# Kernel optimization log

Measured on AMD Instinct MI355X. Metric: run time of the kernel, lower is better.

The kernel has to match this reference:

```python
import jax, jax.numpy as jnp
import numpy as np
import math

N = 50000
E = 500000
IN_C = 128
T_FEAT = 16
OUT_C = 128
EPS = 1e-5
NEG_SLOPE = 0.01


def setup_inputs() -> dict:
    key = jax.random.key(0)
    ks = jax.random.split(key, 10)
    x = jax.random.normal(ks[0], (N, IN_C), dtype=jnp.float32)
    edge_index = jax.random.randint(ks[1], (2, E), 0, N, dtype=jnp.int64)
    edge_weight = jax.random.uniform(ks[2], (E,), dtype=jnp.float32)
    time_diff = jax.random.uniform(ks[3], (1,), dtype=jnp.float32)
    d_in = IN_C + T_FEAT
    morning_freq = jax.random.normal(ks[4], (T_FEAT,), dtype=jnp.float32)
    W_gcn = jax.random.normal(ks[5], (d_in, OUT_C), dtype=jnp.float32) / np.sqrt(d_in)
    b_gcn = jnp.zeros((OUT_C,), dtype=jnp.float32)
    gamma = jnp.ones((OUT_C,), dtype=jnp.float32)
    beta = jnp.zeros((OUT_C,), dtype=jnp.float32)
    W_lin = jax.random.normal(ks[6], (OUT_C, OUT_C), dtype=jnp.float32) / np.sqrt(OUT_C)
    b_lin = jax.random.normal(ks[7], (OUT_C,), dtype=jnp.float32) * 0.01
    return {"x": x, "edge_index": edge_index, "edge_weight": edge_weight,
            "time_diff": time_diff, "morning_freq": morning_freq,
            "W_gcn": W_gcn, "b_gcn": b_gcn, "gamma": gamma, "beta": beta,
            "W_lin": W_lin, "b_lin": b_lin}


def _gcn_conv(h, edge_index, edge_weight):
    # PyG GCNConv aggregation: add self-loops (weight 1), symmetric normalization.
    row, col = edge_index[0], edge_index[1]
    loop = jnp.arange(N, dtype=edge_index.dtype)
    row_f = jnp.concatenate([row, loop])
    col_f = jnp.concatenate([col, loop])
    ew_f = jnp.concatenate([edge_weight, jnp.ones((N,), dtype=h.dtype)])
    deg = jax.ops.segment_sum(ew_f, col_f, num_segments=N)
    dinv = jnp.where(deg > 0, jax.lax.rsqrt(jnp.maximum(deg, 1e-12)), 0.0)
    norm = dinv[row_f] * ew_f * dinv[col_f]                 # [E+N]
    msg = h[row_f] * norm[:, None]                          # gather + scale
    return jax.ops.segment_sum(msg, col_f, num_segments=N)  # scatter-add


def reference(x, edge_index, edge_weight, time_diff, morning_freq,
              W_gcn, b_gcn, gamma, beta, W_lin, b_lin):
    td = time_diff[0]
    # time_segment == 'morning_peak': sin encoding, tiled over all nodes
    enc = jnp.sin(td * morning_freq * math.pi)              # [T]
    enc = jnp.broadcast_to(enc[None, :], (x.shape[0], T_FEAT))
    h = jnp.concatenate([x, enc], axis=1)                   # [N, in+T]
    h = h @ W_gcn                                           # GCN linear transform
    h = _gcn_conv(h, edge_index, edge_weight) + b_gcn       # [N, out]
    # BatchNorm1d (training-mode batch statistics, biased variance)
    mean = jnp.mean(h, axis=0)
    var = jnp.mean(jnp.square(h - mean), axis=0)
    h = gamma * (h - mean) * jax.lax.rsqrt(var + EPS) + beta
    h = jnp.where(h >= 0, h, NEG_SLOPE * h)                 # LeakyReLU
    h = h @ W_lin + b_lin                                   # Linear (dropout=eval identity)
    return h
```

## Files before the change

### kernel.cpp

```cpp
#include <hip/hip_runtime.h>
#include <hip/hip_bf16.h>

#define NN 50000
#define NE 500000
#define C 128
#define NBLK ((NN + 255) / 256)
#define SPB (NN / 8)
#define RB 128
#define RROWS ((SPB + RB - 1) / RB)
#define BN_EPS 1e-5f
#define NEG 0.01f
#define WSCALE 16777216.0f
#define WMASK  0xFFFFFFFFFFFULL

__device__ inline unsigned short f2bf(float f) {
    unsigned int u = __float_as_uint(f);
    unsigned int r = (u + 0x7fffu + ((u >> 16) & 1u)) >> 16;
    return (unsigned short)r;
}
__device__ inline float4 bf4_to_f4(uint2 u) {
    float4 r;
    r.x = __uint_as_float(u.x << 16);
    r.y = __uint_as_float(u.x & 0xffff0000u);
    r.z = __uint_as_float(u.y << 16);
    r.w = __uint_as_float(u.y & 0xffff0000u);
    return r;
}

__global__ void zero_kernel(float* __restrict__ p, long n) {
    long i = (long)blockIdx.x * blockDim.x + threadIdx.x;
    long s = (long)gridDim.x * blockDim.x;
    for (; i < n; i += s) p[i] = 0.f;
}

__global__ void cvec_kernel(const float* __restrict__ td, const float* __restrict__ mf,
                            const float* __restrict__ Wg, float* __restrict__ cvec) {
    int o = threadIdx.x;
    float t = td[0];
    float acc = 0.f;
#pragma unroll
    for (int j = 0; j < 16; j++) {
        float s = sinf(t * mf[j] * 3.14159265358979323846f);
        acc = fmaf(s, Wg[(128 + j) * C + o], acc);
    }
    cvec[o] = acc;
}

__global__ __launch_bounds__(256) void gemm1_kernel(const float* __restrict__ X,
                                                    const float* __restrict__ W,
                                                    const float* __restrict__ cvec,
                                                    unsigned short* __restrict__ Hb) {
    __shared__ __align__(16) float At[32][68];
    __shared__ __align__(16) float Bt[32][68];
    const int t = threadIdx.x;
    const int r0 = blockIdx.x * 64;
    const int c0 = blockIdx.y * 64;
    const int tr = t >> 4, tc = t & 15;
    float acc[4][4] = {};
    for (int k0 = 0; k0 < 128; k0 += 32) {
#pragma unroll
        for (int rr = 0; rr < 64; rr += 32) {
            int lr = rr + (t >> 3);
            int r = r0 + lr;
            int kk = (t & 7) * 4;
            float4 v = make_float4(0.f, 0.f, 0.f, 0.f);
            if (r < NN) v = *(const float4*)(X + (size_t)r * C + k0 + kk);
            At[kk + 0][lr] = v.x; At[kk + 1][lr] = v.y;
            At[kk + 2][lr] = v.z; At[kk + 3][lr] = v.w;
        }
#pragma unroll
        for (int kk2 = 0; kk2 < 32; kk2 += 16) {
            int k = kk2 + (t >> 4);
            int c = (t & 15) * 4;
            *(float4*)&Bt[k][c] = *(const float4*)(W + (size_t)(k0 + k) * C + c0 + c);
        }
        __syncthreads();
#pragma unroll
        for (int k = 0; k < 32; k++) {
            float4 a = *(const float4*)&At[k][tr * 4];
            float4 b = *(const float4*)&Bt[k][tc * 4];
            float av[4] = {a.x, a.y, a.z, a.w};
            float bv[4] = {b.x, b.y, b.z, b.w};
#pragma unroll
            for (int i = 0; i < 4; i++)
#pragma unroll
                for (int j = 0; j < 4; j++)
                    acc[i][j] = fmaf(av[i], bv[j], acc[i][j]);
        }
        __syncthreads();
    }
    float4 cv = *(const float4*)(cvec + c0 + tc * 4);
#pragma unroll
    for (int i = 0; i < 4; i++) {
        int r = r0 + tr * 4 + i;
        if (r < NN) {
            uint2 o;
            o.x = (unsigned int)f2bf(acc[i][0] + cv.x) | ((unsigned int)f2bf(acc[i][1] + cv.y) << 16);
            o.y = (unsigned int)f2bf(acc[i][2] + cv.z) | ((unsigned int)f2bf(acc[i][3] + cv.w) << 16);
            *(uint2*)(Hb + (size_t)r * C + c0 + tc * 4) = o;
        }
    }
}

__global__ void hist_kernel(const int* __restrict__ ei, const float* __restrict__ ew,
                            unsigned long long* __restrict__ hist) {
    int e = blockIdx.x * blockDim.x + threadIdx.x;
    if (e < NE) {
        int c = ei[NE + e];
        unsigned long long pack = (1ULL << 44) | (unsigned long long)(ew[e] * WSCALE);
        atomicAdd(&hist[c], pack);
    }
}

__global__ __launch_bounds__(256) void scanp1_kernel(const unsigned long long* __restrict__ hist,
                                                     int* __restrict__ rptr,
                                                     int* __restrict__ bsum) {
    __shared__ int s[256];
    const int t = threadIdx.x;
    const int i = blockIdx.x * 256 + t;
    int v = (i < NN) ? (int)(hist[i] >> 44) : 0;
    s[t] = v;
    __syncthreads();
    for (int off = 1; off < 256; off <<= 1) {
        int add = (t >= off) ? s[t - off] : 0;
        __syncthreads();
        s[t] += add;
        __syncthreads();
    }
    if (i < NN) rptr[i] = s[t] - v;
    if (t == 255) bsum[blockIdx.x] = s[255];
}

__global__ __launch_bounds__(256) void scanp2_kernel(const int* __restrict__ bsum,
                                                     int* __restrict__ boff) {
    __shared__ int s[256];
    const int t = threadIdx.x;
    int v = (t < NBLK) ? bsum[t] : 0;
    s[t] = v;
    __syncthreads();
    for (int off = 1; off < 256; off <<= 1) {
        int add = (t >= off) ? s[t - off] : 0;
        __syncthreads();
        s[t] += add;
        __syncthreads();
    }
    if (t < NBLK) boff[t] = s[t] - v;
}

__global__ void scanp3_kernel(int* __restrict__ rptr, const int* __restrict__ boff,
                              const unsigned long long* __restrict__ hist,
                              int* __restrict__ cursor, float* __restrict__ dinv) {
    int i = blockIdx.x * blockDim.x + threadIdx.x;
    if (i < NN) {
        int rp = rptr[i] + boff[i >> 8];
        rptr[i] = rp;
        cursor[i] = rp;
        float degw = (float)(hist[i] & WMASK) * (1.0f / WSCALE);
        dinv[i] = rsqrtf(degw + 1.0f);
    }
    if (i == 0) rptr[NN] = NE;
}

__global__ void fill_kernel(const int* __restrict__ ei, const float* __restrict__ ew,
                            const float* __restrict__ dinv,
                            int* __restrict__ cursor, int2* __restrict__ csr) {
    int e = blockIdx.x * blockDim.x + threadIdx.x;
    if (e >= NE) return;
    int r = ei[e], c = ei[NE + e];
    int slot = atomicAdd(&cursor[c], 1);
    float w = dinv[r] * ew[e] * dinv[c];
    csr[slot] = make_int2(r, __float_as_int(w));
}

__global__ __launch_bounds__(256) void spmm_kernel(const int* __restrict__ rptr,
                                                   const int2* __restrict__ csr,
                                                   const unsigned short* __restrict__ Hb,
                                                   const float* __restrict__ dinv,
                                                   const float* __restrict__ bg,
                                                   float* __restrict__ OUT,
                                                   float* __restrict__ P) {
    const int nl = threadIdx.x >> 5;
    const int lane = threadIdx.x & 31;
    const int node = blockIdx.x * 8 + nl;
    const int ch = lane * 4;
    int s = rptr[node], e = rptr[node + 1];
    float d = dinv[node];
    float dd = d * d;
    float4 h = bf4_to_f4(*(const uint2*)(Hb + (size_t)node * C + ch));
    float4 acc = make_float4(dd * h.x, dd * h.y, dd * h.z, dd * h.w);
    int j = s;
    for (; j + 2 <= e; j += 2) {
        int2 e0 = csr[j], e1 = csr[j + 1];
        float w0 = __int_as_float(e0.y), w1 = __int_as_float(e1.y);
        float4 v0 = bf4_to_f4(*(const uint2*)(Hb + (size_t)e0.x * C + ch));
        float4 v1 = bf4_to_f4(*(const uint2*)(Hb + (size_t)e1.x * C + ch));
        acc.x = fmaf(v0.x, w0, acc.x); acc.y = fmaf(v0.y, w0, acc.y);
        acc.z = fmaf(v0.z, w0, acc.z); acc.w = fmaf(v0.w, w0, acc.w);
        acc.x = fmaf(v1.x, w1, acc.x); acc.y = fmaf(v1.y, w1, acc.y);
        acc.z = fmaf(v1.z, w1, acc.z); acc.w = fmaf(v1.w, w1, acc.w);
    }
    if (j < e) {
        int2 e0 = csr[j];
        float w0 = __int_as_float(e0.y);
        float4 v0 = bf4_to_f4(*(const uint2*)(Hb + (size_t)e0.x * C + ch));
        acc.x = fmaf(v0.x, w0, acc.x); acc.y = fmaf(v0.y, w0, acc.y);
        acc.z = fmaf(v0.z, w0, acc.z); acc.w = fmaf(v0.w, w0, acc.w);
    }
    float4 b = *(const float4*)(bg + ch);
    acc.x += b.x; acc.y += b.y; acc.z += b.z; acc.w += b.w;
    *(float4*)(OUT + (size_t)node * C + ch) = acc;

    __shared__ __align__(16) float4 sred[2][8][32];
    float4 sq = make_float4(acc.x * acc.x, acc.y * acc.y, acc.z * acc.z, acc.w * acc.w);
    sred[0][nl][lane] = acc;
    sred[1][nl][lane] = sq;
    __syncthreads();
    if (nl == 0) {
        float4 s0 = sred[0][0][lane], q0 = sred[1][0][lane];
#pragma unroll
        for (int k = 1; k < 8; k++) {
            float4 a = sred[0][k][lane];
            float4 q = sred[1][k][lane];
            s0.x += a.x; s0.y += a.y; s0.z += a.z; s0.w += a.w;
            q0.x += q.x; q0.y += q.y; q0.z += q.z; q0.w += q.w;
        }
        float* row = P + (size_t)blockIdx.x * 256;
        *(float4*)(row + ch) = s0;
        *(float4*)(row + 128 + ch) = q0;
    }
}

__global__ __launch_bounds__(256) void reduce1_kernel(const float* __restrict__ P,
                                                      float* __restrict__ P2) {
    const int c = threadIdx.x;
    const int r0 = blockIdx.x * RROWS;
    const int r1 = min(r0 + RROWS, SPB);
    float a0 = 0.f, a1 = 0.f, a2 = 0.f, a3 = 0.f;
    int r = r0;
    for (; r + 4 <= r1; r += 4) {
        a0 += P[(size_t)(r + 0) * 256 + c];
        a1 += P[(size_t)(r + 1) * 256 + c];
        a2 += P[(size_t)(r + 2) * 256 + c];
        a3 += P[(size_t)(r + 3) * 256 + c];
    }
    for (; r < r1; r++) a0 += P[(size_t)r * 256 + c];
    P2[(size_t)blockIdx.x * 256 + c] = (a0 + a1) + (a2 + a3);
}

__global__ void bnparam_kernel(const float* __restrict__ P2,
                               const float* __restrict__ gm, const float* __restrict__ bt,
                               float* __restrict__ sc, float* __restrict__ sh) {
    int c = threadIdx.x;
    float s0 = 0.f, s1 = 0.f, q0 = 0.f, q1 = 0.f;
    for (int k = 0; k < RB; k += 2) {
        s0 += P2[(size_t)k * 256 + c];
        q0 += P2[(size_t)k * 256 + 128 + c];
        s1 += P2[(size_t)(k + 1) * 256 + c];
        q1 += P2[(size_t)(k + 1) * 256 + 128 + c];
    }
    float ssum = s0 + s1, ssq = q0 + q1;
    float mean = ssum / (float)NN;
    float var = ssq / (float)NN - mean * mean;
    var = fmaxf(var, 0.f);
    float r = rsqrtf(var + BN_EPS);
    float s = gm[c] * r;
    sc[c] = s;
    sh[c] = bt[c] - mean * s;
}

__global__ __launch_bounds__(256) void final_kernel(float* __restrict__ OUT,
                                                    const float* __restrict__ WL,
                                                    const float* __restrict__ bl,
                                                    const float* __restrict__ sc,
                                                    const float* __restrict__ sh) {
    __shared__ __align__(16) float At[32][68];
    __shared__ __align__(16) float Bt[32][132];
    const int t = threadIdx.x;
    const int r0 = blockIdx.x * 64;
    const int tr = t >> 4, tc = t & 15;
    float acc[4][8] = {};
    for (int k0 = 0; k0 < 128; k0 += 32) {
#pragma unroll
        for (int rr = 0; rr < 64; rr += 32) {
            int lr = rr + (t >> 3);
            int r = r0 + lr;
            int kk = (t & 7) * 4;
            float4 v = make_float4(0.f, 0.f, 0.f, 0.f);
            if (r < NN) v = *(const float4*)(OUT + (size_t)r * C + k0 + kk);
            float4 s4 = *(const float4*)(sc + k0 + kk);
            float4 h4 = *(const float4*)(sh + k0 + kk);
            float a0 = fmaf(v.x, s4.x, h4.x); a0 = a0 >= 0.f ? a0 : NEG * a0;
            float a1 = fmaf(v.y, s4.y, h4.y); a1 = a1 >= 0.f ? a1 : NEG * a1;
            float a2 = fmaf(v.z, s4.z, h4.z); a2 = a2 >= 0.f ? a2 : NEG * a2;
            float a3 = fmaf(v.w, s4.w, h4.w); a3 = a3 >= 0.f ? a3 : NEG * a3;
            At[kk + 0][lr] = a0; At[kk + 1][lr] = a1;
            At[kk + 2][lr] = a2; At[kk + 3][lr] = a3;
        }
#pragma unroll
        for (int kk2 = 0; kk2 < 32; kk2 += 8) {
            int k = kk2 + (t >> 5);
            int c = (t & 31) * 4;
            *(float4*)&Bt[k][c] = *(const float4*)(WL + (size_t)(k0 + k) * C + c);
        }
        __syncthreads();
#pragma unroll
        for (int k = 0; k < 32; k++) {
            float4 a = *(const float4*)&At[k][tr * 4];
            float4 b0 = *(const float4*)&Bt[k][tc * 8];
            float4 b1 = *(const float4*)&Bt[k][tc * 8 + 4];
            float av[4] = {a.x, a.y, a.z, a.w};
            float bv[8] = {b0.x, b0.y, b0.z, b0.w, b1.x, b1.y, b1.z, b1.w};
#pragma unroll
            for (int i = 0; i < 4; i++)
#pragma unroll
                for (int j = 0; j < 8; j++)
                    acc[i][j] = fmaf(av[i], bv[j], acc[i][j]);
        }
        __syncthreads();
    }
    float4 bl0 = *(const float4*)(bl + tc * 8);
    float4 bl1 = *(const float4*)(bl + tc * 8 + 4);
#pragma unroll
    for (int i = 0; i < 4; i++) {
        int r = r0 + tr * 4 + i;
        if (r < NN) {
            float4 o0, o1;
            o0.x = acc[i][0] + bl0.x; o0.y = acc[i][1] + bl0.y;
            o0.z = acc[i][2] + bl0.z; o0.w = acc[i][3] + bl0.w;
            o1.x = acc[i][4] + bl1.x; o1.y = acc[i][5] + bl1.y;
            o1.z = acc[i][6] + bl1.z; o1.w = acc[i][7] + bl1.w;
            *(float4*)(OUT + (size_t)r * C + tc * 8) = o0;
            *(float4*)(OUT + (size_t)r * C + tc * 8 + 4) = o1;
        }
    }
}

extern "C" void kernel_launch(void* const* d_in, const int* in_sizes, int n_in,
                              void* d_out, int out_size, void* d_ws, size_t ws_size,
                              hipStream_t stream) {
    const float* x  = (const float*)d_in[0];
    const int*   ei = (const int*)d_in[1];
    const float* ew = (const float*)d_in[2];
    const float* td = (const float*)d_in[3];
    const float* mf = (const float*)d_in[4];
    const float* Wg = (const float*)d_in[5];
    const float* bg = (const float*)d_in[6];
    const float* gm = (const float*)d_in[7];
    const float* bt = (const float*)d_in[8];
    const float* Wl = (const float*)d_in[9];
    const float* bl = (const float*)d_in[10];
    float* out = (float*)d_out;

    unsigned short* h1b = (unsigned short*)d_ws;
    unsigned long long* hist = (unsigned long long*)(h1b + (size_t)NN * C);
    int*   cursor = (int*)(hist + NN);
    float* dinv   = (float*)(cursor + NN);
    float* cvec   = dinv + NN;
    float* sc     = cvec + C;
    float* sh     = sc + C;
    int*   rptr   = (int*)(sh + C);
    int*   bsum   = rptr + NN + 8;
    int*   boff   = bsum + NBLK;
    int2*  csr    = (int2*)(boff + NBLK + 9);
    float* P      = (float*)(csr + NE);
    float* P2     = P + (size_t)SPB * 256;

    zero_kernel<<<128, 256, 0, stream>>>((float*)hist, 2L * NN);
    cvec_kernel<<<1, 128, 0, stream>>>(td, mf, Wg, cvec);
    gemm1_kernel<<<dim3((NN + 63) / 64, 2), 256, 0, stream>>>(x, Wg, cvec, h1b);
    hist_kernel<<<(NE + 255) / 256, 256, 0, stream>>>(ei, ew, hist);
    scanp1_kernel<<<NBLK, 256, 0, stream>>>(hist, rptr, bsum);
    scanp2_kernel<<<1, 256, 0, stream>>>(bsum, boff);
    scanp3_kernel<<<NBLK, 256, 0, stream>>>(rptr, boff, hist, cursor, dinv);
    fill_kernel<<<(NE + 255) / 256, 256, 0, stream>>>(ei, ew, dinv, cursor, csr);
    spmm_kernel<<<SPB, 256, 0, stream>>>(rptr, csr, h1b, dinv, bg, out, P);
    reduce1_kernel<<<RB, 256, 0, stream>>>(P, P2);
    bnparam_kernel<<<1, 128, 0, stream>>>(P2, gm, bt, sc, sh);
    final_kernel<<<(NN + 63) / 64, 256, 0, stream>>>(out, Wl, bl, sc, sh);
}
```

Before: 173.5 us.

## Use bf16 MFMA for both dense GEMMs and replace fill atomics with hist ranks

Replaces the scalar FP32 SIMT GEMMs (node feature transform and final linear layer) with bf16 MFMA 16x16x32 kernels. The weights are pre-packed once into a swizzled bf16 layout that each block loads whole into shared memory. Separately, the histogram atomic now returns each edge's rank within its destination, so the CSR fill computes its slot directly instead of doing a second atomic on a cursor array. This trades FP32 accuracy in both GEMMs for bf16 inputs and adds a rank array plus a small weight-prep kernel.

```diff
diff --git a/kernel.cpp b/kernel.cpp
--- a/kernel.cpp
+++ b/kernel.cpp
@@ -8,15 +8,22 @@
 #define SPB (NN / 8)
 #define RB 128
 #define RROWS ((SPB + RB - 1) / RB)
+#define GB ((NN + 63) / 64)
 #define BN_EPS 1e-5f
 #define NEG 0.01f
 #define WSCALE 16777216.0f
 #define WMASK  0xFFFFFFFFFFFULL
 
+typedef __attribute__((ext_vector_type(8))) short bf16x8;
+typedef __attribute__((ext_vector_type(4))) float f32x4;
+
 __device__ inline unsigned short f2bf(float f) {
     unsigned int u = __float_as_uint(f);
     unsigned int r = (u + 0x7fffu + ((u >> 16) & 1u)) >> 16;
     return (unsigned short)r;
+}
+__device__ inline unsigned int pack2(float a, float b) {
+    return (unsigned int)f2bf(a) | ((unsigned int)f2bf(b) << 16);
 }
 __device__ inline float4 bf4_to_f4(uint2 u) {
     float4 r;
@@ -33,6 +40,23 @@
     for (; i < n; i += s) p[i] = 0.f;
 }
 
+__global__ __launch_bounds__(256) void wprep_kernel(const float* __restrict__ Wg,
+                                                    const float* __restrict__ Wl,
+                                                    unsigned int* __restrict__ Wgt,
+                                                    unsigned int* __restrict__ Wlt) {
+    const int t = threadIdx.x;
+    const int col = t >> 1;
+    const int half = t & 1;
+    for (int j = 0; j < 32; j++) {
+        int ku = half * 32 + j;
+        int k0 = 2 * ku;
+        unsigned int g = (unsigned int)((ku >> 2) ^ (col & 15));
+        unsigned int slot = (unsigned int)col * 64u + (g << 2) + (unsigned int)(ku & 3);
+        Wgt[slot] = pack2(Wg[(size_t)k0 * C + col], Wg[(size_t)(k0 + 1) * C + col]);
+        Wlt[slot] = pack2(Wl[(size_t)k0 * C + col], Wl[(size_t)(k0 + 1) * C + col]);
+    }
+}
+
 __global__ void cvec_kernel(const float* __restrict__ td, const float* __restrict__ mf,
                             const float* __restrict__ Wg, float* __restrict__ cvec) {
     int o = threadIdx.x;
@@ -47,68 +71,64 @@
 }
 
 __global__ __launch_bounds__(256) void gemm1_kernel(const float* __restrict__ X,
-                                                    const float* __restrict__ W,
+                                                    const unsigned int* __restrict__ Wt,
                                                     const float* __restrict__ cvec,
                                                     unsigned short* __restrict__ Hb) {
-    __shared__ __align__(16) float At[32][68];
-    __shared__ __align__(16) float Bt[32][68];
-    const int t = threadIdx.x;
-    const int r0 = blockIdx.x * 64;
-    const int c0 = blockIdx.y * 64;
-    const int tr = t >> 4, tc = t & 15;
-    float acc[4][4] = {};
-    for (int k0 = 0; k0 < 128; k0 += 32) {
-#pragma unroll
-        for (int rr = 0; rr < 64; rr += 32) {
-            int lr = rr + (t >> 3);
-            int r = r0 + lr;
-            int kk = (t & 7) * 4;
-            float4 v = make_float4(0.f, 0.f, 0.f, 0.f);
-            if (r < NN) v = *(const float4*)(X + (size_t)r * C + k0 + kk);
-            At[kk + 0][lr] = v.x; At[kk + 1][lr] = v.y;
-            At[kk + 2][lr] = v.z; At[kk + 3][lr] = v.w;
-        }
-#pragma unroll
-        for (int kk2 = 0; kk2 < 32; kk2 += 16) {
-            int k = kk2 + (t >> 4);
-            int c = (t & 15) * 4;
-            *(float4*)&Bt[k][c] = *(const float4*)(W + (size_t)(k0 + k) * C + c0 + c);
-        }
-        __syncthreads();
-#pragma unroll
-        for (int k = 0; k < 32; k++) {
-            float4 a = *(const float4*)&At[k][tr * 4];
-            float4 b = *(const float4*)&Bt[k][tc * 4];
-            float av[4] = {a.x, a.y, a.z, a.w};
-            float bv[4] = {b.x, b.y, b.z, b.w};
-#pragma unroll
-            for (int i = 0; i < 4; i++)
-#pragma unroll
-                for (int j = 0; j < 4; j++)
-                    acc[i][j] = fmaf(av[i], bv[j], acc[i][j]);
-        }
-        __syncthreads();
-    }
-    float4 cv = *(const float4*)(cvec + c0 + tc * 4);
-#pragma unroll
-    for (int i = 0; i < 4; i++) {
-        int r = r0 + tr * 4 + i;
-        if (r < NN) {
-            uint2 o;
-            o.x = (unsigned int)f2bf(acc[i][0] + cv.x) | ((unsigned int)f2bf(acc[i][1] + cv.y) << 16);
-            o.y = (unsigned int)f2bf(acc[i][2] + cv.z) | ((unsigned int)f2bf(acc[i][3] + cv.w) << 16);
-            *(uint2*)(Hb + (size_t)r * C + c0 + tc * 4) = o;
+    __shared__ unsigned int wsh[8192];
+    const int t = threadIdx.x;
+#pragma unroll
+    for (int i = 0; i < 8; i++)
+        ((uint4*)wsh)[t + i * 256] = ((const uint4*)Wt)[t + i * 256];
+
+    const int lane = t & 63;
+    const int wid = t >> 6;
+    const int lrow = lane & 15;
+    const int kb = lane >> 4;
+    const int row = blockIdx.x * 64 + wid * 16 + lrow;
+    const float* xrow = X + (size_t)min(row, NN - 1) * C;
+
+    f32x4 acc[8];
+#pragma unroll
+    for (int n = 0; n < 8; n++) acc[n] = (f32x4){0.f, 0.f, 0.f, 0.f};
+    __syncthreads();
+
+#pragma unroll
+    for (int ks = 0; ks < 4; ks++) {
+        float4 a0 = *(const float4*)(xrow + ks * 32 + kb * 8);
+        float4 a1 = *(const float4*)(xrow + ks * 32 + kb * 8 + 4);
+        union { unsigned int u[4]; bf16x8 v; } af;
+        af.u[0] = pack2(a0.x, a0.y); af.u[1] = pack2(a0.z, a0.w);
+        af.u[2] = pack2(a1.x, a1.y); af.u[3] = pack2(a1.z, a1.w);
+        const unsigned int gp = (unsigned int)((ks * 4 + kb) ^ lrow);
+#pragma unroll
+        for (int n = 0; n < 8; n++) {
+            int col = n * 16 + lrow;
+            union { uint4 q; bf16x8 v; } bfm;
+            bfm.q = *(const uint4*)&wsh[col * 64 + gp * 4];
+            acc[n] = __builtin_amdgcn_mfma_f32_16x16x32_bf16(af.v, bfm.v, acc[n], 0, 0, 0);
+        }
+    }
+    const int orow = blockIdx.x * 64 + wid * 16 + kb * 4;
+#pragma unroll
+    for (int n = 0; n < 8; n++) {
+        int col = n * 16 + lrow;
+        float cv = cvec[col];
+#pragma unroll
+        for (int i = 0; i < 4; i++) {
+            int r = orow + i;
+            if (r < NN) Hb[(size_t)r * C + col] = f2bf(acc[n][i] + cv);
         }
     }
 }
 
 __global__ void hist_kernel(const int* __restrict__ ei, const float* __restrict__ ew,
-                            unsigned long long* __restrict__ hist) {
+                            unsigned long long* __restrict__ hist, int* __restrict__ rank) {
     int e = blockIdx.x * blockDim.x + threadIdx.x;
     if (e < NE) {
         int c = ei[NE + e];
         unsigned long long pack = (1ULL << 44) | (unsigned long long)(ew[e] * WSCALE);
-        atomicAdd(&hist[c], pack);
+        unsigned long long old = atomicAdd(&hist[c], pack);
+        rank[e] = (int)(old >> 44);
     }
 }
 
@@ -149,12 +169,10 @@
 
 __global__ void scanp3_kernel(int* __restrict__ rptr, const int* __restrict__ boff,
                               const unsigned long long* __restrict__ hist,
-                              int* __restrict__ cursor, float* __restrict__ dinv) {
+                              float* __restrict__ dinv) {
     int i = blockIdx.x * blockDim.x + threadIdx.x;
     if (i < NN) {
-        int rp = rptr[i] + boff[i >> 8];
-        rptr[i] = rp;
-        cursor[i] = rp;
+        rptr[i] += boff[i >> 8];
         float degw = (float)(hist[i] & WMASK) * (1.0f / WSCALE);
         dinv[i] = rsqrtf(degw + 1.0f);
     }
@@ -162,12 +180,12 @@
 }
 
 __global__ void fill_kernel(const int* __restrict__ ei, const float* __restrict__ ew,
-                            const float* __restrict__ dinv,
-                            int* __restrict__ cursor, int2* __restrict__ csr) {
+                            const float* __restrict__ dinv, const int* __restrict__ rptr,
+                            const int* __restrict__ rank, int2* __restrict__ csr) {
     int e = blockIdx.x * blockDim.x + threadIdx.x;
     if (e >= NE) return;
     int r = ei[e], c = ei[NE + e];
-    int slot = atomicAdd(&cursor[c], 1);
+    int slot = rptr[c] + rank[e];
     float w = dinv[r] * ew[e] * dinv[c];
     csr[slot] = make_int2(r, __float_as_int(w));
 }
@@ -269,68 +287,65 @@
 }
 
 __global__ __launch_bounds__(256) void final_kernel(float* __restrict__ OUT,
-                                                    const float* __restrict__ WL,
+                                                    const unsigned int* __restrict__ Wt,
                                                     const float* __restrict__ bl,
                                                     const float* __restrict__ sc,
                                                     const float* __restrict__ sh) {
-    __shared__ __align__(16) float At[32][68];
-    __shared__ __align__(16) float Bt[32][132];
-    const int t = threadIdx.x;
-    const int r0 = blockIdx.x * 64;
-    const int tr = t >> 4, tc = t & 15;
-    float acc[4][8] = {};
-    for (int k0 = 0; k0 < 128; k0 += 32) {
-#pragma unroll
-        for (int rr = 0; rr < 64; rr += 32) {
-            int lr = rr + (t >> 3);
-            int r = r0 + lr;
-            int kk = (t & 7) * 4;
-            float4 v = make_float4(0.f, 0.f, 0.f, 0.f);
-            if (r < NN) v = *(const float4*)(OUT + (size_t)r * C + k0 + kk);
-            float4 s4 = *(const float4*)(sc + k0 + kk);
-            float4 h4 = *(const float4*)(sh + k0 + kk);
-            float a0 = fmaf(v.x, s4.x, h4.x); a0 = a0 >= 0.f ? a0 : NEG * a0;
-            float a1 = fmaf(v.y, s4.y, h4.y); a1 = a1 >= 0.f ? a1 : NEG * a1;
-            float a2 = fmaf(v.z, s4.z, h4.z); a2 = a2 >= 0.f ? a2 : NEG * a2;
-            float a3 = fmaf(v.w, s4.w, h4.w); a3 = a3 >= 0.f ? a3 : NEG * a3;
-            At[kk + 0][lr] = a0; At[kk + 1][lr] = a1;
-            At[kk + 2][lr] = a2; At[kk + 3][lr] = a3;
-        }
-#pragma unroll
-        for (int kk2 = 0; kk2 < 32; kk2 += 8) {
-            int k = kk2 + (t >> 5);
-            int c = (t & 31) * 4;
-            *(float4*)&Bt[k][c] = *(const float4*)(WL + (size_t)(k0 + k) * C + c);
-        }
-        __syncthreads();
-#pragma unroll
-        for (int k = 0; k < 32; k++) {
-            float4 a = *(const float4*)&At[k][tr * 4];
-            float4 b0 = *(const float4*)&Bt[k][tc * 8];
-            float4 b1 = *(const float4*)&Bt[k][tc * 8 + 4];
-            float av[4] = {a.x, a.y, a.z, a.w};
-            float bv[8] = {b0.x, b0.y, b0.z, b0.w, b1.x, b1.y, b1.z, b1.w};
-#pragma unroll
-            for (int i = 0; i < 4; i++)
-#pragma unroll
-                for (int j = 0; j < 8; j++)
-                    acc[i][j] = fmaf(av[i], bv[j], acc[i][j]);
-        }
-        __syncthreads();
-    }
-    float4 bl0 = *(const float4*)(bl + tc * 8);
-    float4 bl1 = *(const float4*)(bl + tc * 8 + 4);
-#pragma unroll
-    for (int i = 0; i < 4; i++) {
-        int r = r0 + tr * 4 + i;
-        if (r < NN) {
-            float4 o0, o1;
-            o0.x = acc[i][0] + bl0.x; o0.y = acc[i][1] + bl0.y;
-            o0.z = acc[i][2] + bl0.z; o0.w = acc[i][3] + bl0.w;
-            o1.x = acc[i][4] + bl1.x; o1.y = acc[i][5] + bl1.y;
-            o1.z = acc[i][6] + bl1.z; o1.w = acc[i][7] + bl1.w;
-            *(float4*)(OUT + (size_t)r * C + tc * 8) = o0;
-            *(float4*)(OUT + (size_t)r * C + tc * 8 + 4) = o1;
+    __shared__ unsigned int wsh[8192];
+    const int t = threadIdx.x;
+#pragma unroll
+    for (int i = 0; i < 8; i++)
+        ((uint4*)wsh)[t + i * 256] = ((const uint4*)Wt)[t + i * 256];
+
+    const int lane = t & 63;
+    const int wid = t >> 6;
+    const int lrow = lane & 15;
+    const int kb = lane >> 4;
+    const int row = blockIdx.x * 64 + wid * 16 + lrow;
+    const float* hrow = OUT + (size_t)min(row, NN - 1) * C;
+
+    f32x4 acc[8];
+#pragma unroll
+    for (int n = 0; n < 8; n++) acc[n] = (f32x4){0.f, 0.f, 0.f, 0.f};
+    __syncthreads();
+
+#pragma unroll
+    for (int ks = 0; ks < 4; ks++) {
+        const int k0 = ks * 32 + kb * 8;
+        float4 v0 = *(const float4*)(hrow + k0);
+        float4 v1 = *(const float4*)(hrow + k0 + 4);
+        float4 s0 = *(const float4*)(sc + k0);
+        float4 s1 = *(const float4*)(sc + k0 + 4);
+        float4 h0 = *(const float4*)(sh + k0);
+        float4 h1 = *(const float4*)(sh + k0 + 4);
+        float a[8];
+        a[0] = fmaf(v0.x, s0.x, h0.x); a[1] = fmaf(v0.y, s0.y, h0.y);
+        a[2] = fmaf(v0.z, s0.z, h0.z); a[3] = fmaf(v0.w, s0.w, h0.w);
+        a[4] = fmaf(v1.x, s1.x, h1.x); a[5] = fmaf(v1.y, s1.y, h1.y);
+        a[6] = fmaf(v1.z, s1.z, h1.z); a[7] = fmaf(v1.w, s1.w, h1.w);
+#pragma unroll
+        for (int i = 0; i < 8; i++) a[i] = a[i] >= 0.f ? a[i] : NEG * a[i];
+        union { unsigned int u[4]; bf16x8 v; } af;
+        af.u[0] = pack2(a[0], a[1]); af.u[1] = pack2(a[2], a[3]);
+        af.u[2] = pack2(a[4], a[5]); af.u[3] = pack2(a[6], a[7]);
+        const unsigned int gp = (unsigned int)((ks * 4 + kb) ^ lrow);
+#pragma unroll
+        for (int n = 0; n < 8; n++) {
+            int col = n * 16 + lrow;
+            union { uint4 q; bf16x8 v; } bfm;
+            bfm.q = *(const uint4*)&wsh[col * 64 + gp * 4];
+            acc[n] = __builtin_amdgcn_mfma_f32_16x16x32_bf16(af.v, bfm.v, acc[n], 0, 0, 0);
+        }
+    }
+    const int orow = blockIdx.x * 64 + wid * 16 + kb * 4;
+#pragma unroll
+    for (int n = 0; n < 8; n++) {
+        int col = n * 16 + lrow;
+        float blv = bl[col];
+#pragma unroll
+        for (int i = 0; i < 4; i++) {
+            int r = orow + i;
+            if (r < NN) OUT[(size_t)r * C + col] = acc[n][i] + blv;
         }
     }
 }
@@ -353,28 +368,31 @@
 
     unsigned short* h1b = (unsigned short*)d_ws;
     unsigned long long* hist = (unsigned long long*)(h1b + (size_t)NN * C);
-    int*   cursor = (int*)(hist + NN);
-    float* dinv   = (float*)(cursor + NN);
+    float* dinv   = (float*)(hist + NN);
     float* cvec   = dinv + NN;
     float* sc     = cvec + C;
     float* sh     = sc + C;
     int*   rptr   = (int*)(sh + C);
     int*   bsum   = rptr + NN + 8;
     int*   boff   = bsum + NBLK;
-    int2*  csr    = (int2*)(boff + NBLK + 9);
+    int*   rank   = boff + NBLK + 8;
+    int2*  csr    = (int2*)(rank + NE);
     float* P      = (float*)(csr + NE);
     float* P2     = P + (size_t)SPB * 256;
+    unsigned int* Wgt = (unsigned int*)(P2 + RB * 256);
+    unsigned int* Wlt = Wgt + 8192;
 
     zero_kernel<<<128, 256, 0, stream>>>((float*)hist, 2L * NN);
+    wprep_kernel<<<1, 256, 0, stream>>>(Wg, Wl, Wgt, Wlt);
     cvec_kernel<<<1, 128, 0, stream>>>(td, mf, Wg, cvec);
-    gemm1_kernel<<<dim3((NN + 63) / 64, 2), 256, 0, stream>>>(x, Wg, cvec, h1b);
-    hist_kernel<<<(NE + 255) / 256, 256, 0, stream>>>(ei, ew, hist);
+    gemm1_kernel<<<GB, 256, 0, stream>>>(x, Wgt, cvec, h1b);
+    hist_kernel<<<(NE + 255) / 256, 256, 0, stream>>>(ei, ew, hist, rank);
     scanp1_kernel<<<NBLK, 256, 0, stream>>>(hist, rptr, bsum);
     scanp2_kernel<<<1, 256, 0, stream>>>(bsum, boff);
-    scanp3_kernel<<<NBLK, 256, 0, stream>>>(rptr, boff, hist, cursor, dinv);
-    fill_kernel<<<(NE + 255) / 256, 256, 0, stream>>>(ei, ew, dinv, cursor, csr);
+    scanp3_kernel<<<NBLK, 256, 0, stream>>>(rptr, boff, hist, dinv);
+    fill_kernel<<<(NE + 255) / 256, 256, 0, stream>>>(ei, ew, dinv, rptr, rank, csr);
     spmm_kernel<<<SPB, 256, 0, stream>>>(rptr, csr, h1b, dinv, bg, out, P);
     reduce1_kernel<<<RB, 256, 0, stream>>>(P, P2);
     bnparam_kernel<<<1, 128, 0, stream>>>(P2, gm, bt, sc, sh);
-    final_kernel<<<(NN + 63) / 64, 256, 0, stream>>>(out, Wl, bl, sc, sh);
-}
+    final_kernel<<<GB, 256, 0, stream>>>(out, Wlt, bl, sc, sh);
+}
```

Result: faster. 147.9 us (-14.8%).
